# Kernel tuning notes

Hardware: AMD Instinct MI355X
Metric: run time of the kernel (lower is better)

Reference implementation:

```python
import jax, jax.numpy as jnp
import numpy as np

B, S, K, N = 4, 2048, 4096, 4096


def setup_inputs() -> dict:
    key = jax.random.key(0)
    k1, k2, k3, k4 = jax.random.split(key, 4)
    x = jax.random.normal(k1, (B, S, K), dtype=jnp.float32)
    # int8 quantized weight values in [-128, 127], stored as int32 (jax-friendly container)
    qw = jax.random.randint(k2, (N, K), -128, 128, dtype=jnp.int32)
    # per-tensor scale: amax/127 style scalar
    sw = (jax.random.uniform(k3, (), dtype=jnp.float32) * 0.02 + 0.001)
    bias = jax.random.normal(k4, (N,), dtype=jnp.float32)
    return {"x": x, "qw": qw, "sw": sw, "bias": bias}


def reference(x, qw, sw, bias):
    # per_tensor_matmul: dequantize weight to fp32 with scalar scale, fp32 GEMM, cast back, add bias
    x_dtype = x.dtype
    w = qw.astype(jnp.float32) * sw          # [N, K] dequantized
    y = jnp.einsum('bsk,nk->bsn', x.astype(jnp.float32), w).astype(x_dtype)
    y = y + bias                              # [B, S, N]
    return y
```

## Files before the change

### kernel.cpp

```cpp
#include <hip/hip_runtime.h>
#include <stdint.h>

#define MDIM 8192
#define NDIM 4096
#define KDIM 4096

#define BM 256
#define BN 256
#define BK 128
#define NKT (KDIM / BK)

typedef __attribute__((ext_vector_type(4)))  int i32x4;

#define AS1 __attribute__((address_space(1)))
#define AS3 __attribute__((address_space(3)))

__device__ __forceinline__ int clamp127(int v) {
    return v > 127 ? 127 : (v < -127 ? -127 : v);
}

__global__ __launch_bounds__(256) void quant_x(
        const float* __restrict__ x, const float* __restrict__ sw,
        int8_t* __restrict__ Aq, float* __restrict__ scales) {
    const int row = blockIdx.x;
    const int t   = threadIdx.x;
    const float4* px = (const float4*)(x + (size_t)row * KDIM);

    float4 v[4];
#pragma unroll
    for (int j = 0; j < 4; j++) v[j] = px[t + 256 * j];

    float a = 0.f;
#pragma unroll
    for (int j = 0; j < 4; j++) {
        a = fmaxf(a, fabsf(v[j].x)); a = fmaxf(a, fabsf(v[j].y));
        a = fmaxf(a, fabsf(v[j].z)); a = fmaxf(a, fabsf(v[j].w));
    }
#pragma unroll
    for (int off = 32; off >= 1; off >>= 1)
        a = fmaxf(a, __shfl_xor(a, off));
    __shared__ float red[4];
    if ((t & 63) == 0) red[t >> 6] = a;
    __syncthreads();
    const float amax = fmaxf(fmaxf(red[0], red[1]), fmaxf(red[2], red[3]));
    const float inv  = (amax > 0.f) ? (127.0f / amax) : 0.f;
    if (t == 0) scales[row] = (amax * (1.0f / 127.0f)) * (*sw);

    int* out32 = (int*)(Aq + (size_t)row * KDIM);
#pragma unroll
    for (int j = 0; j < 4; j++) {
        int b0 = clamp127(__float2int_rn(v[j].x * inv));
        int b1 = clamp127(__float2int_rn(v[j].y * inv));
        int b2 = clamp127(__float2int_rn(v[j].z * inv));
        int b3 = clamp127(__float2int_rn(v[j].w * inv));
        out32[t + 256 * j] = (b0 & 255) | ((b1 & 255) << 8) | ((b2 & 255) << 16) | ((b3 & 255) << 24);
    }
}

__global__ __launch_bounds__(256) void cvt_w(const int* __restrict__ qw, int8_t* __restrict__ Bq) {
    const long i = (long)blockIdx.x * 256 + threadIdx.x;
    int4 a = ((const int4*)qw)[i];
    ((int*)Bq)[i] = (a.x & 255) | ((a.y & 255) << 8) | ((a.z & 255) << 16) | ((a.w & 255) << 24);
}


#define BAR()    do { asm volatile("" ::: "memory"); __builtin_amdgcn_s_barrier(); asm volatile("" ::: "memory"); } while (0)
#define LGKM0()  asm volatile("s_waitcnt lgkmcnt(0)" ::: "memory")
#define WAITV(n) asm volatile("s_waitcnt vmcnt(" #n ")" ::: "memory")

#define STAGE_A(buf, h, kt) do { \
    __builtin_amdgcn_global_load_lds((AS1 const void*)(gA + (size_t)((h) * 128) * KDIM + (kt) * 128), \
        (AS3 void*)(sA + (buf) * 32768 + (h) * 16384 + sdst), 16, 0, 0); \
    __builtin_amdgcn_global_load_lds((AS1 const void*)(gA + (size_t)((h) * 128 + 64) * KDIM + (kt) * 128), \
        (AS3 void*)(sA + (buf) * 32768 + (h) * 16384 + 8192 + sdst), 16, 0, 0); \
} while (0)

#define STAGE_B(buf, h, kt) do { \
    __builtin_amdgcn_global_load_lds((AS1 const void*)(gB + (size_t)((h) * 128) * KDIM + (kt) * 128), \
        (AS3 void*)(sB + (buf) * 32768 + (h) * 16384 + sdst), 16, 0, 0); \
    __builtin_amdgcn_global_load_lds((AS1 const void*)(gB + (size_t)((h) * 128 + 64) * KDIM + (kt) * 128), \
        (AS3 void*)(sB + (buf) * 32768 + (h) * 16384 + 8192 + sdst), 16, 0, 0); \
} while (0)

#define READ_A0(buf) do { \
    _Pragma("unroll") for (int mi = 0; mi < 4; ++mi) \
    _Pragma("unroll") for (int ks = 0; ks < 2; ++ks) \
        aF0[mi][ks] = *(const i32x4*)(sA + (buf) * 32768 + rbA + mi * 2048 + co[ks]); \
} while (0)

#define READ_A1(buf) do { \
    _Pragma("unroll") for (int mi = 0; mi < 4; ++mi) \
    _Pragma("unroll") for (int ks = 0; ks < 2; ++ks) \
        aF1[mi][ks] = *(const i32x4*)(sA + (buf) * 32768 + rbA + (4 + mi) * 2048 + co[ks]); \
} while (0)

#define READ_B01(buf) do { \
    _Pragma("unroll") for (int ni = 0; ni < 2; ++ni) \
    _Pragma("unroll") for (int ks = 0; ks < 2; ++ks) \
        bF01[ni][ks] = *(const i32x4*)(sB + (buf) * 32768 + rbB + ni * 2048 + co[ks]); \
} while (0)

#define READ_B23(buf) do { \
    _Pragma("unroll") for (int ni = 0; ni < 2; ++ni) \
    _Pragma("unroll") for (int ks = 0; ks < 2; ++ks) \
        bF23[ni][ks] = *(const i32x4*)(sB + (buf) * 32768 + rbB + (2 + ni) * 2048 + co[ks]); \
} while (0)

#define MMA_(AF, accbase, BF, nhofs) do { \
    __builtin_amdgcn_s_setprio(1); \
    _Pragma("unroll") for (int ks = 0; ks < 2; ++ks) \
    _Pragma("unroll") for (int mi = 0; mi < 4; ++mi) \
    _Pragma("unroll") for (int nj = 0; nj < 2; ++nj) \
        acc[(accbase) + mi][(nhofs) + nj] = __builtin_amdgcn_mfma_i32_16x16x64_i8( \
            AF[mi][ks], BF[nj][ks], acc[(accbase) + mi][(nhofs) + nj], 0, 0, 0); \
    __builtin_amdgcn_s_setprio(0); \
} while (0)

__global__ __launch_bounds__(512, 2) void gemm_bt_i8(
        const int8_t* __restrict__ A,
        const int8_t* __restrict__ Bm,
        const float* __restrict__ scales,
        const float* __restrict__ bias,
        float* __restrict__ C)
{
    __shared__ __align__(16) int8_t sA[2 * BM * BK];
    __shared__ __align__(16) int8_t sB[2 * BN * BK];

    const int tid  = threadIdx.x;
    const int wave = tid >> 6;
    const int lane = tid & 63;
    const int wr   = wave >> 2;
    const int wc   = wave & 3;
    const int lr   = lane & 15;
    const int lg   = lane >> 4;

    const int orig = blockIdx.y * 16 + blockIdx.x;
    const int nu   = (orig & 7) * 64 + (orig >> 3);
    const int m0   = (nu >> 4) * BM;
    const int n0   = (nu & 15) * BN;

    const int trow = tid >> 3;
    const int slog = (tid & 7) ^ ((tid >> 3) & 7);
    const int8_t* gA = A  + (size_t)(m0 + trow) * KDIM + slog * 16;
    const int8_t* gB = Bm + (size_t)(n0 + trow) * KDIM + slog * 16;
    const int sdst = tid * 16;

    const int f3 = lr & 7;
    const int rbA = (wr * 128 + lr) * BK;
    const int rbB = (wc * 64  + lr) * BK;
    int co[2];
#pragma unroll
    for (int ks = 0; ks < 2; ++ks) co[ks] = (((ks << 2) | lg) ^ f3) << 4;

    i32x4 acc[8][4];
#pragma unroll
    for (int mi = 0; mi < 8; ++mi)
#pragma unroll
        for (int ni = 0; ni < 4; ++ni)
#pragma unroll
            for (int r = 0; r < 4; ++r) acc[mi][ni][r] = 0;

    i32x4 aF0[4][2];
    i32x4 aF1[4][2];
    i32x4 bF01[2][2];
    i32x4 bF23[2][2];

    STAGE_A(0, 0, 0); STAGE_A(0, 1, 0);
    STAGE_B(0, 0, 0); STAGE_B(0, 1, 0);
    STAGE_A(1, 0, 1); STAGE_A(1, 1, 1);
    WAITV(4);
    BAR();
    READ_A0(0); READ_B01(0);

#pragma unroll 1
    for (int it = 0; it < NKT / 2 - 1; ++it) {
        const int e = 2 * it;
        READ_A1(0);                 MMA_(aF0, 0, bF01, 0); STAGE_B(1, 0, e + 1); BAR();
        READ_B23(0);                MMA_(aF1, 4, bF01, 0); STAGE_B(1, 1, e + 1); LGKM0(); BAR();
                                    MMA_(aF0, 0, bF23, 2); STAGE_A(0, 0, e + 2); WAITV(2); BAR();
        READ_A0(1); READ_B01(1);    MMA_(aF1, 4, bF23, 2); STAGE_A(0, 1, e + 2); BAR();
        READ_A1(1);                 MMA_(aF0, 0, bF01, 0); STAGE_B(0, 0, e + 2); BAR();
        READ_B23(1);                MMA_(aF1, 4, bF01, 0); STAGE_B(0, 1, e + 2); LGKM0(); BAR();
                                    MMA_(aF0, 0, bF23, 2); STAGE_A(1, 0, e + 3); WAITV(2); BAR();
        READ_A0(0); READ_B01(0);    MMA_(aF1, 4, bF23, 2); STAGE_A(1, 1, e + 3); BAR();
    }

    READ_A1(0);                 MMA_(aF0, 0, bF01, 0); STAGE_B(1, 0, 31); BAR();
    READ_B23(0);                MMA_(aF1, 4, bF01, 0); STAGE_B(1, 1, 31); LGKM0(); BAR();
                                MMA_(aF0, 0, bF23, 2); WAITV(0); BAR();
    READ_A0(1); READ_B01(1);    MMA_(aF1, 4, bF23, 2); BAR();
    READ_A1(1);                 MMA_(aF0, 0, bF01, 0); BAR();
    READ_B23(1);                MMA_(aF1, 4, bF01, 0); BAR();
                                MMA_(aF0, 0, bF23, 2);
                                MMA_(aF1, 4, bF23, 2);

#pragma unroll
    for (int mi = 0; mi < 8; ++mi) {
        const int row_base = m0 + wr * 128 + mi * 16 + lg * 4;
        float sc[4];
#pragma unroll
        for (int r = 0; r < 4; ++r) sc[r] = scales[row_base + r];
#pragma unroll
        for (int ni = 0; ni < 4; ++ni) {
            const int col = n0 + wc * 64 + ni * 16 + lr;
            const float bc = bias[col];
#pragma unroll
            for (int r = 0; r < 4; ++r)
                C[(size_t)(row_base + r) * NDIM + col] = (float)acc[mi][ni][r] * sc[r] + bc;
        }
    }
}

__global__ void gemm_naive_f32(const float* __restrict__ x, const int* __restrict__ qw,
                               const float* __restrict__ sw, const float* __restrict__ bias,
                               float* __restrict__ out) {
    size_t id = (size_t)blockIdx.x * blockDim.x + threadIdx.x;
    if (id >= (size_t)MDIM * NDIM) return;
    int m = (int)(id / NDIM);
    int n = (int)(id % NDIM);
    const float* xr = x + (size_t)m * KDIM;
    const int*   wr = qw + (size_t)n * KDIM;
    float acc = 0.f;
    for (int k = 0; k < KDIM; k++) acc += xr[k] * (float)wr[k];
    out[id] = acc * (*sw) + bias[n];
}

extern "C" void kernel_launch(void* const* d_in, const int* in_sizes, int n_in,
                              void* d_out, int out_size, void* d_ws, size_t ws_size,
                              hipStream_t stream) {
    const float* x    = (const float*)d_in[0];
    const int*   qw   = (const int*)d_in[1];
    const float* sw   = (const float*)d_in[2];
    const float* bias = (const float*)d_in[3];
    float* out = (float*)d_out;

    const size_t needA = (size_t)MDIM * KDIM;
    const size_t needB = (size_t)NDIM * KDIM;
    const size_t needS = (size_t)MDIM * sizeof(float);

    if (ws_size >= needA + needB + needS) {
        int8_t* Aq = (int8_t*)d_ws;
        int8_t* Bq = Aq + needA;
        float*  scales = (float*)(Bq + needB);

        quant_x<<<MDIM, 256, 0, stream>>>(x, sw, Aq, scales);
        const long nw4 = (long)NDIM * KDIM / 4;
        cvt_w<<<(int)(nw4 / 256), 256, 0, stream>>>(qw, Bq);

        dim3 grid(NDIM / BN, MDIM / BM);
        gemm_bt_i8<<<grid, 512, 0, stream>>>(Aq, Bq, scales, bias, out);
    } else {
        size_t total = (size_t)MDIM * NDIM;
        gemm_naive_f32<<<(total + 255) / 256, 256, 0, stream>>>(x, qw, sw, bias, out);
    }
}
```

Baseline: 399.7 us.

## Restructure int8 GEMM main loop schedule with two-barrier ping-pong phases

Reorders the software pipeline of the int8 MFMA main loop. The prologue now stages the B tile for k-step 1 instead of A. Each phase issues LDS reads and a global-to-LDS stage, waits on partial lgkm counts, then runs its MMA between two barriers, in a ping-pong style. The aim is to separate LDS reads from MFMA work across waves and overlap memory traffic with compute. The cost is twice as many barriers per phase, plus changed wait counts that risk stalls or races.

```diff
diff --git a/kernel.cpp b/kernel.cpp
--- a/kernel.cpp
+++ b/kernel.cpp
@@ -66,6 +66,7 @@
 
 #define BAR()    do { asm volatile("" ::: "memory"); __builtin_amdgcn_s_barrier(); asm volatile("" ::: "memory"); } while (0)
 #define LGKM0()  asm volatile("s_waitcnt lgkmcnt(0)" ::: "memory")
+#define LGKM8()  asm volatile("s_waitcnt lgkmcnt(8)" ::: "memory")
 #define WAITV(n) asm volatile("s_waitcnt vmcnt(" #n ")" ::: "memory")
 
 #define STAGE_A(buf, h, kt) do { \
@@ -167,32 +168,31 @@
 
     STAGE_A(0, 0, 0); STAGE_A(0, 1, 0);
     STAGE_B(0, 0, 0); STAGE_B(0, 1, 0);
-    STAGE_A(1, 0, 1); STAGE_A(1, 1, 1);
+    STAGE_B(1, 0, 1); STAGE_B(1, 1, 1);
     WAITV(4);
     BAR();
-    READ_A0(0); READ_B01(0);
 
 #pragma unroll 1
     for (int it = 0; it < NKT / 2 - 1; ++it) {
-        const int e = 2 * it;
-        READ_A1(0);                 MMA_(aF0, 0, bF01, 0); STAGE_B(1, 0, e + 1); BAR();
-        READ_B23(0);                MMA_(aF1, 4, bF01, 0); STAGE_B(1, 1, e + 1); LGKM0(); BAR();
-                                    MMA_(aF0, 0, bF23, 2); STAGE_A(0, 0, e + 2); WAITV(2); BAR();
-        READ_A0(1); READ_B01(1);    MMA_(aF1, 4, bF23, 2); STAGE_A(0, 1, e + 2); BAR();
-        READ_A1(1);                 MMA_(aF0, 0, bF01, 0); STAGE_B(0, 0, e + 2); BAR();
-        READ_B23(1);                MMA_(aF1, 4, bF01, 0); STAGE_B(0, 1, e + 2); LGKM0(); BAR();
-                                    MMA_(aF0, 0, bF23, 2); STAGE_A(1, 0, e + 3); WAITV(2); BAR();
-        READ_A0(0); READ_B01(0);    MMA_(aF1, 4, bF23, 2); STAGE_A(1, 1, e + 3); BAR();
-    }
-
-    READ_A1(0);                 MMA_(aF0, 0, bF01, 0); STAGE_B(1, 0, 31); BAR();
-    READ_B23(0);                MMA_(aF1, 4, bF01, 0); STAGE_B(1, 1, 31); LGKM0(); BAR();
-                                MMA_(aF0, 0, bF23, 2); WAITV(0); BAR();
-    READ_A0(1); READ_B01(1);    MMA_(aF1, 4, bF23, 2); BAR();
-    READ_A1(1);                 MMA_(aF0, 0, bF01, 0); BAR();
-    READ_B23(1);                MMA_(aF1, 4, bF01, 0); BAR();
-                                MMA_(aF0, 0, bF23, 2);
-                                MMA_(aF1, 4, bF23, 2);
+        const int o = 2 * it + 1, e2 = 2 * it + 2, o2 = 2 * it + 3;
+        READ_A0(0); READ_B01(0); STAGE_A(1, 0, o);  LGKM8(); BAR(); LGKM0(); MMA_(aF0, 0, bF01, 0); BAR();
+        READ_B23(0);             STAGE_A(1, 1, o);           BAR(); LGKM0(); MMA_(aF0, 0, bF23, 2); BAR();
+        READ_A1(0);              STAGE_B(0, 0, e2);          BAR(); LGKM0(); MMA_(aF1, 4, bF23, 2); BAR();
+                                 STAGE_B(0, 1, e2); WAITV(4); BAR();         MMA_(aF1, 4, bF01, 0); BAR();
+        READ_A0(1); READ_B01(1); STAGE_A(0, 0, e2); LGKM8(); BAR(); LGKM0(); MMA_(aF0, 0, bF01, 0); BAR();
+        READ_B23(1);             STAGE_A(0, 1, e2);          BAR(); LGKM0(); MMA_(aF0, 0, bF23, 2); BAR();
+        READ_A1(1);              STAGE_B(1, 0, o2);          BAR(); LGKM0(); MMA_(aF1, 4, bF23, 2); BAR();
+                                 STAGE_B(1, 1, o2); WAITV(4); BAR();         MMA_(aF1, 4, bF01, 0); BAR();
+    }
+
+    READ_A0(0); READ_B01(0); STAGE_A(1, 0, 31); LGKM8(); BAR(); LGKM0(); MMA_(aF0, 0, bF01, 0); BAR();
+    READ_B23(0);             STAGE_A(1, 1, 31);          BAR(); LGKM0(); MMA_(aF0, 0, bF23, 2); BAR();
+    READ_A1(0);                                          BAR(); LGKM0(); MMA_(aF1, 4, bF23, 2); BAR();
+                             WAITV(0);                   BAR();          MMA_(aF1, 4, bF01, 0); BAR();
+    READ_A0(1); READ_B01(1); LGKM8();                    BAR(); LGKM0(); MMA_(aF0, 0, bF01, 0); BAR();
+    READ_B23(1);                                         BAR(); LGKM0(); MMA_(aF0, 0, bF23, 2); BAR();
+    READ_A1(1);                                                 LGKM0(); MMA_(aF1, 4, bF23, 2);
+    MMA_(aF1, 4, bF01, 0);
 
 #pragma unroll
     for (int mi = 0; mi < 8; ++mi) {
```

New measurement: 388.0 us. 2.9% less time.
